# Performance work log

Hardware: AMD Instinct MI355X
Metric: run time of the kernel (lower is better)

The kernel has to match this reference:

```python
import jax, jax.numpy as jnp
import numpy as np

B = 65536
G = 9          # grid_size
C = 10         # num_classes
BS = 3         # block_size = sqrt(grid_size)
CONSTRAINT_WEIGHT = 0.1


def setup_inputs() -> dict:
    key = jax.random.key(0)
    k1, k2, k3 = jax.random.split(key, 3)
    logits = jax.random.normal(k1, (B, G, G, C), dtype=jnp.float32)
    targets = jax.random.randint(k2, (B, G, G), 0, C)
    puzzles = jax.random.randint(k3, (B, G, G), 0, C)
    return {"logits": logits, "targets": targets, "puzzles": puzzles}


def _sudoku_loss(logits, targets, puzzles):
    mask = (puzzles == 0).astype(logits.dtype)               # [B, G, G]

    # --- masked cross-entropy over empty cells ---
    logp = jax.nn.log_softmax(logits, axis=-1)               # [B, G, G, C]
    ce = -jnp.take_along_axis(logp, targets[..., None], axis=-1)[..., 0]
    ce_loss = (ce * mask).sum() / (mask.sum() + 1e-8)

    # --- constraint loss (rows, cols, 3x3 boxes), fully vectorized ---
    probs = jnp.exp(logp)                                    # softmax probs
    wp = probs * mask[..., None]                             # [B, G, G, C]

    def group_mse(digit_sums, msum):
        # digit_sums: [B, G_groups, C]; msum: [B, G_groups]
        # torch: per-group F.mse_loss over [B, C-1], summed over groups
        target = msum[..., None] / G                         # [B, Gg, 1]
        diff = digit_sums[..., 1:] - target                  # [B, Gg, C-1]
        return (diff * diff).mean(axis=(0, 2)).sum()

    # rows: sum over columns (axis 2)
    row_loss = group_mse(wp.sum(axis=2), mask.sum(axis=2))
    # cols: sum over rows (axis 1)
    col_loss = group_mse(wp.sum(axis=1), mask.sum(axis=1))
    # boxes: reshape to [B, bi, ri, bj, cj, C], sum within-box dims
    box_ds = wp.reshape(B, BS, BS, BS, BS, C).sum(axis=(2, 4)).reshape(B, G, C)
    box_ms = mask.reshape(B, BS, BS, BS, BS).sum(axis=(2, 4)).reshape(B, G)
    box_loss = group_mse(box_ds, box_ms)

    num_constraints = G * 2 + BS * BS                        # 27
    constraint_loss = (row_loss + col_loss + box_loss) / num_constraints

    # torch wraps the constraint loss in torch.tensor(...), detaching it
    total = ce_loss + CONSTRAINT_WEIGHT * jax.lax.stop_gradient(constraint_loss)
    return total, ce_loss, constraint_loss


def reference(logits, targets, puzzles):
    total, ce_loss, constraint_loss = _sudoku_loss(logits, targets, puzzles)
    return total, ce_loss, constraint_loss
```

## Files before the change

### kernel.cpp

```cpp
#include <hip/hip_runtime.h>


constexpr int kB    = 65536;
constexpr int PPB   = 6;
constexpr int TPB   = 512;
constexpr int NSLOT = 256;
constexpr int SLOT_STRIDE = 16;

__global__ __launch_bounds__(TPB) void sudoku_main(
    const float* __restrict__ logits,
    const int*   __restrict__ targets,
    const int*   __restrict__ puzzles,
    float*       __restrict__ ws)
{
    __shared__ float acc[PPB * 270];
    __shared__ float red[3][TPB / 64];

    const int tid = threadIdx.x;
    for (int i = tid; i < PPB * 270; i += TPB) acc[i] = 0.f;
    __syncthreads();

    const int pzbase = blockIdx.x * PPB;
    const int q      = tid / 81;
    const int ci     = tid - q * 81;

    float ce = 0.f, mcnt = 0.f, diff2 = 0.f;

    if (q < PPB && (pzbase + q) < kB) {
        const int idx = pzbase * 81 + tid;
        const int pz = puzzles[idx];
        const int tg = targets[idx];

        if (pz == 0) {
            const float* xp = logits + (size_t)idx * 10;
            float x[10];
            #pragma unroll
            for (int h = 0; h < 5; ++h) {
                const float2 v = *(const float2*)(xp + 2 * h);
                x[2 * h] = v.x; x[2 * h + 1] = v.y;
            }
            float mx = x[0];
            #pragma unroll
            for (int c = 1; c < 10; ++c) mx = fmaxf(mx, x[c]);
            float e[10];
            float S = 0.f;
            #pragma unroll
            for (int c = 0; c < 10; ++c) { e[c] = __expf(x[c] - mx); S += e[c]; }
            const float inv = 1.0f / S;

            float xt = x[0];
            #pragma unroll
            for (int c = 1; c < 10; ++c) xt = (tg == c) ? x[c] : xt;
            ce   = mx + __logf(S) - xt;
            mcnt = 1.f;

            const int r  = ci / 9;
            const int j  = ci - r * 9;
            const int bx = (r / 3) * 3 + (j / 3);
            float* a = &acc[q * 270];
            float* ar = a + r * 10;
            float* ac = a + (9 + j) * 10;
            float* ab = a + (18 + bx) * 10;
            atomicAdd(ar + 9, 1.f);
            atomicAdd(ac + 9, 1.f);
            atomicAdd(ab + 9, 1.f);
            #pragma unroll
            for (int c = 1; c < 10; ++c) {
                const float w = e[c] * inv;
                atomicAdd(ar + (c - 1), w);
                atomicAdd(ac + (c - 1), w);
                atomicAdd(ab + (c - 1), w);
            }
        }
    }
    __syncthreads();

    if (tid < PPB * 27) {
        const float* a = &acc[tid * 10];
        const float tm = a[9] * (1.f / 9.f);
        #pragma unroll
        for (int c = 0; c < 9; ++c) { const float d = a[c] - tm; diff2 += d * d; }
    }

    #pragma unroll
    for (int off = 32; off > 0; off >>= 1) {
        diff2 += __shfl_down(diff2, off);
        ce    += __shfl_down(ce, off);
        mcnt  += __shfl_down(mcnt, off);
    }
    const int wave = tid >> 6;
    if ((tid & 63) == 0) { red[0][wave] = diff2; red[1][wave] = ce; red[2][wave] = mcnt; }
    __syncthreads();
    if (tid == 0) {
        float d = 0.f, c2 = 0.f, m = 0.f;
        #pragma unroll
        for (int w = 0; w < TPB / 64; ++w) { d += red[0][w]; c2 += red[1][w]; m += red[2][w]; }
        float* slot = ws + (size_t)(blockIdx.x & (NSLOT - 1)) * SLOT_STRIDE;
        atomicAdd(&slot[0], d);
        atomicAdd(&slot[1], c2);
        atomicAdd(&slot[2], m);
    }
}

__global__ void sudoku_final(const float* __restrict__ ws, float* __restrict__ out)
{
    const int t = threadIdx.x;
    float d = 0.f, c2 = 0.f, m = 0.f;
    for (int s = t; s < NSLOT; s += 64) {
        const float* sl = ws + (size_t)s * SLOT_STRIDE;
        d += sl[0]; c2 += sl[1]; m += sl[2];
    }
    #pragma unroll
    for (int off = 32; off > 0; off >>= 1) {
        d  += __shfl_down(d, off);
        c2 += __shfl_down(c2, off);
        m  += __shfl_down(m, off);
    }
    if (t == 0) {
        const float ce_loss = c2 / (m + 1e-8f);
        const float constraint = d / ((float)kB * 9.f * 27.f);
        out[0] = ce_loss + 0.1f * constraint;
        out[1] = ce_loss;
        out[2] = constraint;
    }
}

extern "C" void kernel_launch(void* const* d_in, const int* in_sizes, int n_in,
                              void* d_out, int out_size, void* d_ws, size_t ws_size,
                              hipStream_t stream)
{
    const float* logits  = (const float*)d_in[0];
    const int*   targets = (const int*)d_in[1];
    const int*   puzzles = (const int*)d_in[2];
    float* ws  = (float*)d_ws;
    float* out = (float*)d_out;

    hipMemsetAsync(d_ws, 0, NSLOT * SLOT_STRIDE * sizeof(float), stream);

    const int blocks = (kB + PPB - 1) / PPB;
    sudoku_main<<<blocks, TPB, 0, stream>>>(logits, targets, puzzles, ws);
    sudoku_final<<<1, 64, 0, stream>>>(ws, out);
}
```

Measured before the change: 364.9 us.

## Replace LDS atomic group accumulation with per-cell prob staging and gather sums

```diff
diff --git a/kernel.cpp b/kernel.cpp
--- a/kernel.cpp
+++ b/kernel.cpp
@@ -6,6 +6,7 @@
 constexpr int TPB   = 512;
 constexpr int NSLOT = 256;
 constexpr int SLOT_STRIDE = 16;
+constexpr int CSTRIDE = 12;
 
 __global__ __launch_bounds__(TPB) void sudoku_main(
     const float* __restrict__ logits,
@@ -13,73 +14,114 @@
     const int*   __restrict__ puzzles,
     float*       __restrict__ ws)
 {
-    __shared__ float acc[PPB * 270];
+    __shared__ __align__(16) float probs[TPB * CSTRIDE];
     __shared__ float red[3][TPB / 64];
 
-    const int tid = threadIdx.x;
-    for (int i = tid; i < PPB * 270; i += TPB) acc[i] = 0.f;
-    __syncthreads();
-
+    const int tid    = threadIdx.x;
     const int pzbase = blockIdx.x * PPB;
     const int q      = tid / 81;
-    const int ci     = tid - q * 81;
 
-    float ce = 0.f, mcnt = 0.f, diff2 = 0.f;
+    float ce = 0.f, mcnt = 0.f;
+    float wv[10];
+    #pragma unroll
+    for (int c = 0; c < 10; ++c) wv[c] = 0.f;
 
-    if (q < PPB && (pzbase + q) < kB) {
+    const bool active = (q < PPB) && (pzbase + q < kB);
+    if (active) {
         const int idx = pzbase * 81 + tid;
         const int pz = puzzles[idx];
         const int tg = targets[idx];
 
+        const float* xp = logits + (size_t)idx * 10;
+        float x[10];
+        #pragma unroll
+        for (int h = 0; h < 5; ++h) {
+            const float2 v = *(const float2*)(xp + 2 * h);
+            x[2 * h] = v.x; x[2 * h + 1] = v.y;
+        }
+        float mx = x[0];
+        #pragma unroll
+        for (int c = 1; c < 10; ++c) mx = fmaxf(mx, x[c]);
+        float e[10];
+        float S = 0.f;
+        #pragma unroll
+        for (int c = 0; c < 10; ++c) { e[c] = __expf(x[c] - mx); S += e[c]; }
+        const float inv = 1.0f / S;
+
         if (pz == 0) {
-            const float* xp = logits + (size_t)idx * 10;
-            float x[10];
-            #pragma unroll
-            for (int h = 0; h < 5; ++h) {
-                const float2 v = *(const float2*)(xp + 2 * h);
-                x[2 * h] = v.x; x[2 * h + 1] = v.y;
-            }
-            float mx = x[0];
-            #pragma unroll
-            for (int c = 1; c < 10; ++c) mx = fmaxf(mx, x[c]);
-            float e[10];
-            float S = 0.f;
-            #pragma unroll
-            for (int c = 0; c < 10; ++c) { e[c] = __expf(x[c] - mx); S += e[c]; }
-            const float inv = 1.0f / S;
-
             float xt = x[0];
             #pragma unroll
             for (int c = 1; c < 10; ++c) xt = (tg == c) ? x[c] : xt;
             ce   = mx + __logf(S) - xt;
             mcnt = 1.f;
-
-            const int r  = ci / 9;
-            const int j  = ci - r * 9;
-            const int bx = (r / 3) * 3 + (j / 3);
-            float* a = &acc[q * 270];
-            float* ar = a + r * 10;
-            float* ac = a + (9 + j) * 10;
-            float* ab = a + (18 + bx) * 10;
-            atomicAdd(ar + 9, 1.f);
-            atomicAdd(ac + 9, 1.f);
-            atomicAdd(ab + 9, 1.f);
+            wv[0] = 1.f;
             #pragma unroll
-            for (int c = 1; c < 10; ++c) {
-                const float w = e[c] * inv;
-                atomicAdd(ar + (c - 1), w);
-                atomicAdd(ac + (c - 1), w);
-                atomicAdd(ab + (c - 1), w);
-            }
+            for (int c = 1; c < 10; ++c) wv[c] = e[c] * inv;
         }
+    }
+    {
+        float* dst = &probs[tid * CSTRIDE];
+        *(float4*)(dst + 0) = make_float4(wv[0], wv[1], wv[2], wv[3]);
+        *(float4*)(dst + 4) = make_float4(wv[4], wv[5], wv[6], wv[7]);
+        *(float2*)(dst + 8) = make_float2(wv[8], wv[9]);
     }
     __syncthreads();
 
+    float diff2 = 0.f;
     if (tid < PPB * 27) {
-        const float* a = &acc[tid * 10];
-        const float tm = a[9] * (1.f / 9.f);
+        float s[10];
         #pragma unroll
-        for (int c = 0; c < 9; ++c) { const float d = a[c] - tm; diff2 += d * d; }
+        for (int c = 0; c < 10; ++c) s[c] = 0.f;
+
+        if (tid < PPB * 9) {
+            const int q2 = tid / 9, r = tid - q2 * 9;
+            const float* base = &probs[(q2 * 81 + r * 9) * CSTRIDE];
+            #pragma unroll
+            for (int i = 0; i < 9; ++i) {
+                const float* cell = base + i * CSTRIDE;
+                const float4 a = *(const float4*)(cell + 0);
+                const float4 b = *(const float4*)(cell + 4);
+                const float2 c2 = *(const float2*)(cell + 8);
+                s[0]+=a.x; s[1]+=a.y; s[2]+=a.z; s[3]+=a.w;
+                s[4]+=b.x; s[5]+=b.y; s[6]+=b.z; s[7]+=b.w;
+                s[8]+=c2.x; s[9]+=c2.y;
+            }
+        } else if (tid < PPB * 18) {
+            const int u = tid - PPB * 9;
+            const int q2 = u / 9, j = u - q2 * 9;
+            const float* base = &probs[(q2 * 81 + j) * CSTRIDE];
+            #pragma unroll
+            for (int i = 0; i < 9; ++i) {
+                const float* cell = base + i * (9 * CSTRIDE);
+                const float4 a = *(const float4*)(cell + 0);
+                const float4 b = *(const float4*)(cell + 4);
+                const float2 c2 = *(const float2*)(cell + 8);
+                s[0]+=a.x; s[1]+=a.y; s[2]+=a.z; s[3]+=a.w;
+                s[4]+=b.x; s[5]+=b.y; s[6]+=b.z; s[7]+=b.w;
+                s[8]+=c2.x; s[9]+=c2.y;
+            }
+        } else {
+            const int u = tid - PPB * 18;
+            const int q2 = u / 9, b = u - q2 * 9;
+            const int br = b / 3, bc = b - br * 3;
+            const float* base = &probs[(q2 * 81 + br * 27 + bc * 3) * CSTRIDE];
+            #pragma unroll
+            for (int dr = 0; dr < 3; ++dr) {
+                #pragma unroll
+                for (int dc = 0; dc < 3; ++dc) {
+                    const float* cell = base + (dr * 9 + dc) * CSTRIDE;
+                    const float4 a = *(const float4*)(cell + 0);
+                    const float4 bb = *(const float4*)(cell + 4);
+                    const float2 c2 = *(const float2*)(cell + 8);
+                    s[0]+=a.x; s[1]+=a.y; s[2]+=a.z; s[3]+=a.w;
+                    s[4]+=bb.x; s[5]+=bb.y; s[6]+=bb.z; s[7]+=bb.w;
+                    s[8]+=c2.x; s[9]+=c2.y;
+                }
+            }
+        }
+        const float tm = s[0] * (1.f / 9.f);
+        #pragma unroll
+        for (int c = 1; c < 10; ++c) { const float d = s[c] - tm; diff2 += d * d; }
     }
 
     #pragma unroll
```

After: 351.7 us. 1.04x faster.
